# Kernel optimization log

Hardware: AMD Instinct MI355X
Metric: run time of the kernel (lower is better)

Reference implementation:

```python
import jax, jax.numpy as jnp
import numpy as np

B = 2
NUM_CLS = 20
NUM_DIM = 256
H = W = 448
FH = FW = 28
K_TOP = 25


def _l2norm(x, eps=1e-12):
    # matches torch F.normalize(dim=1): x / max(||x||, eps); zero rows stay zero
    return x / jnp.maximum(jnp.linalg.norm(x, axis=-1, keepdims=True), eps)


def setup_inputs():
    key = jax.random.key(0)
    k1, k2, k3, k4 = jax.random.split(key, 4)
    fmap = jax.random.normal(k1, (B, NUM_DIM, FH, FW), jnp.float32)
    cam = jax.random.uniform(k2, (B, NUM_CLS, H, W), jnp.float32)
    cls_label = jax.random.randint(k3, (B, NUM_CLS), 0, 2).astype(jnp.float32)
    proj_weight = jax.random.normal(k4, (NUM_CLS, NUM_DIM), jnp.float32) * 0.02
    feature_contrast = jnp.zeros((NUM_CLS, NUM_DIM), jnp.float32)
    return {"fmap": fmap, "cam": cam, "cls_label": cls_label,
            "proj_weight": proj_weight, "feature_contrast": feature_contrast,
            "hig_thre": 0.7, "low_thre": 0.25, "bg_thre": 0.5}


def _forward(fmap, cam, cls_label, proj_weight, feature_contrast, hig_thre, low_thre, bg_thre):
    b, c, h, w = cam.shape
    d = fmap.shape[1]
    dt = fmap.dtype

    # ---- pseudo-label generation (vectorized over b,h,w) ----
    valid_cam = cls_label[:, :, None, None] * cam                       # [B,C,H,W]
    top2_v, top2_i = jax.lax.top_k(jnp.moveaxis(valid_cam, 1, -1), 2)   # [B,H,W,2]
    top1, second = top2_v[..., 0], top2_v[..., 1]
    pseudo = top2_i[..., 0] + 1
    pseudo = jnp.where(top1 < hig_thre, 255, pseudo)
    pseudo = jnp.where(top1 < low_thre, 0, pseudo)
    pseudo = jnp.where(top1 < bg_thre, 0, pseudo)
    pseudo = jnp.where((top1 - second < 0.3) & (top1 > hig_thre), 255, pseudo)

    # ---- upsample features (bilinear, align_corners=False) ----
    fmap_up = jax.image.resize(fmap, (b, d, h, w), 'bilinear')
    fmap_flat = fmap_up.reshape(b, d, h * w)                            # [B,D,HW]
    pseudo_flat = pseudo.reshape(b, h * w)                              # [B,HW]

    # ---- per-class features, both branches computed densely then selected ----
    cls_ids = jnp.arange(c) + 1
    mask = (pseudo_flat[:, None, :] == cls_ids[None, :, None]).astype(dt)  # [B,C,HW]
    counts = mask.sum(-1)                                                  # [B,C]
    feat_mask = jnp.einsum('bcp,bdp->bcd', mask, fmap_flat) / jnp.maximum(counts, 1.0)[:, :, None]
    _, top_idx = jax.lax.top_k(valid_cam.reshape(b, c, h * w), K_TOP)      # [B,C,25]
    gathered = jnp.take_along_axis(fmap_flat[:, None, :, :], top_idx[:, :, None, :], axis=-1)  # [B,C,D,25]
    feat_topk = gathered.mean(-1)                                          # [B,C,D]
    present = cls_label > 0.5                                              # [B,C] bool
    fsm = jnp.where((counts == 0.0)[:, :, None], feat_topk, feat_mask) * present[:, :, None]

    eye_f = jnp.eye(c, dtype=dt)
    eye_b = jnp.eye(c, dtype=bool)

    # ---- sequential per-sample loop (EMA memory bank carried across batch) ----
    def step(carry, xs):
        fc, loss_cls, loss_ccf = carry
        fsm_i, present_i = xs                                    # [C,D], [C]
        fsm_n = _l2norm(fsm_i)
        fc_n = _l2norm(jax.lax.stop_gradient(fc))
        cos = jnp.clip(jnp.abs(fsm_n @ fc_n.T), 1e-5, 1.0 - 1e-5)  # [C,C]
        ident = jnp.diag(present_i.astype(dt))
        loss_ccf = loss_ccf - (ident * jnp.log(cos) + (1.0 - ident) * jnp.log1p(-cos)).mean()
        off_max = jnp.where(eye_b, -jnp.inf, cos).max(axis=1)      # max over j != c
        qualify = present_i & (off_max < 0.6)                      # [C] bool
        p = jax.nn.softmax(fsm_i @ proj_weight.T, axis=-1)         # [C,C]
        logp = jnp.maximum(jnp.log(p), -100.0)
        log1mp = jnp.maximum(jnp.log1p(-p), -100.0)
        term = -(eye_f * logp + (1.0 - eye_f) * log1mp).mean(axis=-1)  # BCE(softmax, onehot) per class
        loss_cls = loss_cls + jnp.sum(jnp.where(qualify, term, 0.0))
        n = qualify.sum().astype(dt)
        loss_cls = jnp.where(n > 0, loss_cls / jnp.maximum(n, 1.0), loss_cls)
        fc = jnp.where(qualify[:, None], 0.95 * fc + 0.05 * jax.lax.stop_gradient(fsm_i), fc)
        return (fc, loss_cls, loss_ccf), None

    zero = jnp.asarray(0.0, dt)
    (_, loss_cls, loss_ccf), _ = jax.lax.scan(step, (feature_contrast, zero, zero), (fsm, present))
    return loss_ccf + loss_cls


def reference(fmap, cam, cls_label, proj_weight, feature_contrast, hig_thre, low_thre, bg_thre):
    return _forward(fmap, cam, cls_label, proj_weight, feature_contrast, hig_thre, low_thre, bg_thre)
```

## Files before the change

### kernel.cpp

```cpp
#include <hip/hip_runtime.h>
#include <cstdint>

#define HW 200704
#define IMG_W 448
#define NCLS 20
#define NDIM 256
#define NB2 784
#define LK 260

#define ASYNC_COPY4(gp, lp)                                                    \
  __builtin_amdgcn_global_load_lds(                                            \
      (const __attribute__((address_space(1))) void*)(gp),                     \
      (__attribute__((address_space(3))) void*)(lp), 4, 0, 0)

__global__ __launch_bounds__(256) void k_front(const float* __restrict__ fmap,
                                               float* __restrict__ fmapT,
                                               const float* __restrict__ cam,
                                               const float* __restrict__ cls_label,
                                               const float* __restrict__ hig_p,
                                               const float* __restrict__ low_p,
                                               const float* __restrict__ bg_p,
                                               float* __restrict__ W) {
  __shared__ float sT[NCLS][256];
  int tid = threadIdx.x;

  if (blockIdx.x >= 2 * NB2) {
    float (*tile)[33] = (float (*)[33]) & sT[0][0];
    int blk = blockIdx.x - 2 * NB2;
    int b = blk / 200;
    int t = blk % 200;
    int dT = t / 25, sT2 = t % 25;
    int ty = tid >> 5, tx = tid & 31;
#pragma unroll
    for (int r = 0; r < 4; ++r) {
      int d = dT * 32 + ty + r * 8;
      int s = sT2 * 32 + tx;
      if (s < 784) tile[ty + r * 8][tx] = fmap[((size_t)(b * 256 + d)) * 784 + s];
    }
    __syncthreads();
#pragma unroll
    for (int r = 0; r < 4; ++r) {
      int s = sT2 * 32 + ty + r * 8;
      int d = dT * 32 + tx;
      if (s < 784) fmapT[((size_t)(b * 784 + s)) * 256 + d] = tile[tx][ty + r * 8];
    }
    return;
  }

  int b = blockIdx.x / NB2;
  int blkInB = blockIdx.x % NB2;
  int pix0 = blkInB * 256;
  int wave = tid >> 6, lane = tid & 63;

  bool pres = (lane < NCLS) && (cls_label[b * NCLS + lane] != 0.0f);
  unsigned long long pm = __ballot(pres);
  unsigned mask = (unsigned)(pm & 0xFFFFFu);
  int np = __popc(mask);
  const float* camb = cam + (size_t)b * NCLS * HW + pix0 + wave * 64 + lane;

  {
    unsigned m = mask;
    for (int k = 0; k < np; ++k) {
      int c = __builtin_ctz(m); m &= m - 1u;
      ASYNC_COPY4(camb + (size_t)c * HW, &sT[k][wave * 64]);
    }
  }
  __builtin_amdgcn_s_waitcnt(0);

  float top1 = -1.0f, sec = -1.0f;
  int cls1 = 0;
  {
    unsigned m = mask;
    for (int k = 0; k < np; ++k) {
      int c = __builtin_ctz(m); m &= m - 1u;
      float x = sT[k][tid];
      bool gt = x > top1;
      sec = gt ? top1 : fmaxf(sec, fminf(x, top1));
      cls1 = gt ? c : cls1;
      top1 = gt ? x : top1;
    }
  }
  if (np < NCLS) sec = fmaxf(sec, 0.0f);
  float hig = hig_p[0], low = low_p[0], bg = bg_p[0];
  int pix = pix0 + tid;
  int ps = cls1 + 1;
  if (top1 < hig) ps = 255;
  if (top1 < low) ps = 0;
  if (top1 < bg)  ps = 0;
  if ((top1 - sec < 0.3f) && (top1 > hig)) ps = 255;
  if (ps >= 1 && ps <= NCLS) {
    int cls = ps - 1;
    int y = pix / IMG_W, x = pix % IMG_W;
    float sy = (y + 0.5f) * 0.0625f - 0.5f; sy = fminf(fmaxf(sy, 0.0f), 27.0f);
    float sx = (x + 0.5f) * 0.0625f - 0.5f; sx = fminf(fmaxf(sx, 0.0f), 27.0f);
    int fy0 = (int)sy, fx0 = (int)sx;
    int fy1 = min(fy0 + 1, 27), fx1 = min(fx0 + 1, 27);
    float wy = sy - (float)fy0, wx = sx - (float)fx0;
    float* Wb = W + (size_t)(b * NCLS + cls) * 784;
    atomicAdd(&Wb[fy0 * 28 + fx0], (1.0f - wy) * (1.0f - wx));
    atomicAdd(&Wb[fy0 * 28 + fx1], (1.0f - wy) * wx);
    atomicAdd(&Wb[fy1 * 28 + fx0], wy * (1.0f - wx));
    atomicAdd(&Wb[fy1 * 28 + fx1], wy * wx);
  }
}

__global__ __launch_bounds__(512) void k_feat(const float* __restrict__ fmapT,
                                              const float* __restrict__ cam,
                                              const float* __restrict__ Wg,
                                              const float* __restrict__ cls_label,
                                              float* __restrict__ P,
                                              float* __restrict__ S,
                                              float* __restrict__ cntW) {
  __shared__ float sW[784];
  __shared__ float sH[2][256];
  __shared__ float sRed[8];
  __shared__ float sCntf;
  __shared__ float wv[8]; __shared__ int wi[8];
  __shared__ float selV; __shared__ int selI;
  __shared__ int sTop[25];
  int bc = blockIdx.x >> 2, part = blockIdx.x & 3;
  int b = bc / NCLS;
  int tid = threadIdx.x;
  int dim = tid & 255, h = tid >> 8;
  if (cls_label[bc] == 0.0f) return;

  for (int s = tid; s < 784; s += 512) sW[s] = Wg[(size_t)bc * 784 + s];
  __syncthreads();
  {
    float cs = sW[tid >= 512 ? 0 : tid];
    cs = (tid < 512) ? sW[tid] : 0.0f;
    if (tid < 272) cs += sW[tid + 512];
    for (int off = 32; off > 0; off >>= 1) cs += __shfl_xor(cs, off, 64);
    if ((tid & 63) == 0) sRed[tid >> 6] = cs;
    __syncthreads();
    if (tid == 0) {
      float s = 0.0f;
      for (int w = 0; w < 8; ++w) s += sRed[w];
      sCntf = s;
    }
    __syncthreads();
  }
  float cntf = sCntf;
  const float* fT = fmapT + (size_t)b * 784 * 256;

  if (cntf > 0.0f) {
    int s0 = part * 196;
    if (h == 0) {
      float a0 = 0.0f, a1 = 0.0f;
      for (int s = s0; s < s0 + 196; s += 4) {
        a0 += sW[s]     * fT[(size_t)(s)     * 256 + dim];
        a1 += sW[s + 1] * fT[(size_t)(s + 1) * 256 + dim];
      }
      sH[0][dim] = a0 + a1;
    } else {
      float a2 = 0.0f, a3 = 0.0f;
      for (int s = s0; s < s0 + 196; s += 4) {
        a2 += sW[s + 2] * fT[(size_t)(s + 2) * 256 + dim];
        a3 += sW[s + 3] * fT[(size_t)(s + 3) * 256 + dim];
      }
      sH[1][dim] = a2 + a3;
    }
    __syncthreads();
    if (tid < 256)
      P[(size_t)(bc * 4 + part) * 256 + tid] = sH[0][tid] + sH[1][tid];
    if (part == 0 && tid == 0) cntW[bc] = cntf;
  } else if (part == 0) {
    if (tid == 0) cntW[bc] = 0.0f;
    const float* camc = cam + (size_t)bc * HW;
    float lastV = 3.0e38f; int lastI = -1;
    for (int r = 0; r < 25; ++r) {
      float bv = -1.0e30f; int bi = 0x7fffffff;
      for (int p = tid; p < HW; p += 512) {
        float vv2 = camc[p];
        if (((vv2 < lastV) || (vv2 == lastV && p > lastI)) &&
            ((vv2 > bv) || (vv2 == bv && p < bi))) { bv = vv2; bi = p; }
      }
      for (int off = 32; off > 0; off >>= 1) {
        float ov = __shfl_xor(bv, off, 64);
        int   oi = __shfl_xor(bi, off, 64);
        if (ov > bv || (ov == bv && oi < bi)) { bv = ov; bi = oi; }
      }
      if ((tid & 63) == 0) { wv[tid >> 6] = bv; wi[tid >> 6] = bi; }
      __syncthreads();
      if (tid == 0) {
        for (int w = 1; w < 8; ++w)
          if (wv[w] > bv || (wv[w] == bv && wi[w] < bi)) { bv = wv[w]; bi = wi[w]; }
        selV = bv; selI = bi; sTop[r] = bi;
      }
      __syncthreads();
      lastV = selV; lastI = selI;
    }
    if (tid < 256) {
      float at = 0.0f;
      for (int r = 0; r < 25; ++r) {
        int p = sTop[r];
        int y = p / IMG_W, x = p % IMG_W;
        float sy = (y + 0.5f) * 0.0625f - 0.5f; sy = fminf(fmaxf(sy, 0.0f), 27.0f);
        float sx = (x + 0.5f) * 0.0625f - 0.5f; sx = fminf(fmaxf(sx, 0.0f), 27.0f);
        int fy0 = (int)sy, fx0 = (int)sx;
        int fy1 = min(fy0 + 1, 27), fx1 = min(fx0 + 1, 27);
        float wy = sy - (float)fy0, wx = sx - (float)fx0;
        at += (1.0f - wy) * (1.0f - wx) * fT[(size_t)(fy0 * 28 + fx0) * 256 + tid]
            + (1.0f - wy) * wx          * fT[(size_t)(fy0 * 28 + fx1) * 256 + tid]
            + wy          * (1.0f - wx) * fT[(size_t)(fy1 * 28 + fx0) * 256 + tid]
            + wy          * wx          * fT[(size_t)(fy1 * 28 + fx1) * 256 + tid];
      }
      S[(size_t)bc * 256 + tid] = at * (1.0f / 25.0f);
    }
  }
}

__global__ __launch_bounds__(1024) void k_loss(const float* __restrict__ P,
                                               const float* __restrict__ S,
                                               const float* __restrict__ cntW,
                                               const float* __restrict__ cls_label,
                                               const float* __restrict__ proj_w,
                                               const float* __restrict__ fc_init,
                                               float* __restrict__ out) {
  __shared__ float sFsm[2][NCLS * LK];
  __shared__ float sFc[NCLS * LK], sPw[NCLS * LK];
  __shared__ float sLogit[2][400], sCos[400];
  __shared__ float sBCE[2][NCLS], sRow[NCLS];
  __shared__ float sNormI[2][NCLS], sNormC[NCLS];
  __shared__ int   sZI[2][NCLS], sZC[NCLS], sQual[NCLS];
  __shared__ float sPres[2][NCLS];
  __shared__ float sScal[2];
  int tid = threadIdx.x;

  for (int idx = tid; idx < 2 * NCLS * NDIM; idx += 1024) {
    int bc = idx >> 8, d = idx & 255;
    float v = 0.0f;
    if (cls_label[bc] != 0.0f) {
      float c = cntW[bc];
      if (c > 0.0f) {
        const float* p = P + (size_t)bc * 1024 + d;
        v = ((p[0] + p[256]) + (p[512] + p[768])) / fmaxf(c, 1.0f);
      } else {
        v = S[(size_t)bc * 256 + d];
      }
    }
    sFsm[bc / NCLS][(bc % NCLS) * LK + d] = v;
  }
  for (int idx = tid; idx < NCLS * NDIM; idx += 1024) {
    int r = idx >> 8, d = idx & 255;
    sFc[r * LK + d] = fc_init[idx];
    sPw[r * LK + d] = proj_w[idx];
  }
  if (tid < 40) sPres[tid / NCLS][tid % NCLS] = cls_label[tid];
  if (tid == 0) { sScal[0] = 0.0f; sScal[1] = 0.0f; }
  __syncthreads();

  if (tid < 800) {
    int b = tid / 400, pi = tid % 400;
    int i = pi / NCLS, j = pi % NCLS;
    const float* ra = &sFsm[b][i * LK];
    const float* rb = &sPw[j * LK];
    float a0 = 0, a1 = 0, a2 = 0, a3 = 0, a4 = 0, a5 = 0, a6 = 0, a7 = 0;
    for (int d = 0; d < 256; d += 16) {
      float4 x0 = *(const float4*)&ra[d],      y0 = *(const float4*)&rb[d];
      float4 x1 = *(const float4*)&ra[d + 4],  y1 = *(const float4*)&rb[d + 4];
      float4 x2 = *(const float4*)&ra[d + 8],  y2 = *(const float4*)&rb[d + 8];
      float4 x3 = *(const float4*)&ra[d + 12], y3 = *(const float4*)&rb[d + 12];
      a0 += x0.x * y0.x + x0.y * y0.y;  a1 += x0.z * y0.z + x0.w * y0.w;
      a2 += x1.x * y1.x + x1.y * y1.y;  a3 += x1.z * y1.z + x1.w * y1.w;
      a4 += x2.x * y2.x + x2.y * y2.y;  a5 += x2.z * y2.z + x2.w * y2.w;
      a6 += x3.x * y3.x + x3.y * y3.y;  a7 += x3.z * y3.z + x3.w * y3.w;
    }
    sLogit[b][pi] = ((a0 + a1) + (a2 + a3)) + ((a4 + a5) + (a6 + a7));
  }
  __syncthreads();

  {
    int g = tid >> 3, sub = tid & 7;
    if (g < 60) {
      const float* row = (g < 40) ? &sFsm[g / NCLS][(g % NCLS) * LK] : &sFc[(g - 40) * LK];
      float a0 = 0.0f, a1 = 0.0f, a2 = 0.0f, a3 = 0.0f;
      int d0 = sub * 32;
#pragma unroll
      for (int d = d0; d < d0 + 32; d += 8) {
        float4 x = *(const float4*)&row[d];
        float4 y = *(const float4*)&row[d + 4];
        a0 += x.x * x.x + x.y * x.y;
        a1 += x.z * x.z + x.w * x.w;
        a2 += y.x * y.x + y.y * y.y;
        a3 += y.z * y.z + y.w * y.w;
      }
      float s = (a0 + a1) + (a2 + a3);
      s += __shfl_xor(s, 1, 64);
      s += __shfl_xor(s, 2, 64);
      s += __shfl_xor(s, 4, 64);
      if (sub == 0) {
        if (g < 40) { sNormI[g / NCLS][g % NCLS] = fmaxf(sqrtf(s), 1e-12f); sZI[g / NCLS][g % NCLS] = (s == 0.0f); }
        else { sNormC[g - 40] = fmaxf(sqrtf(s), 1e-12f); sZC[g - 40] = (s == 0.0f); }
      }
    }
  }
  __syncthreads();

  {
    int team = tid >> 5, jj = tid & 31;
    for (int r = team; r < 40; r += 32) {
      int b = r / NCLS, i = r % NCLS;
      float l = (jj < NCLS) ? sLogit[b][i * NCLS + jj] : -3.0e38f;
      float m = l;
#pragma unroll
      for (int off = 1; off < 32; off <<= 1) m = fmaxf(m, __shfl_xor(m, off, 64));
      float e = (jj < NCLS) ? expf(l - m) : 0.0f;
      float sS = e;
#pragma unroll
      for (int off = 1; off < 32; off <<= 1) sS += __shfl_xor(sS, off, 64);
      float term = 0.0f;
      if (jj < NCLS) {
        float p = e / sS;
        term = (jj == i) ? fmaxf(logf(p), -100.0f) : fmaxf(log1pf(-p), -100.0f);
      }
#pragma unroll
      for (int off = 1; off < 32; off <<= 1) term += __shfl_xor(term, off, 64);
      if (jj == 0) sBCE[b][i] = -term / 20.0f;
    }
  }
  __syncthreads();

  for (int b = 0; b < 2; ++b) {
    if (b == 1) {
      int g = tid >> 3, sub = tid & 7;
      if (g < NCLS) {
        const float* row = &sFc[g * LK];
        float a0 = 0.0f, a1 = 0.0f, a2 = 0.0f, a3 = 0.0f;
        int d0 = sub * 32;
#pragma unroll
        for (int d = d0; d < d0 + 32; d += 8) {
          float4 x = *(const float4*)&row[d];
          float4 y = *(const float4*)&row[d + 4];
          a0 += x.x * x.x + x.y * x.y;
          a1 += x.z * x.z + x.w * x.w;
          a2 += y.x * y.x + y.y * y.y;
          a3 += y.z * y.z + y.w * y.w;
        }
        float s = (a0 + a1) + (a2 + a3);
        s += __shfl_xor(s, 1, 64);
        s += __shfl_xor(s, 2, 64);
        s += __shfl_xor(s, 4, 64);
        if (sub == 0) { sNormC[g] = fmaxf(sqrtf(s), 1e-12f); sZC[g] = (s == 0.0f); }
      }
      __syncthreads();
    }
    {
      int pair = tid >> 1, sub = tid & 1;
      if (pair < 400) {
        int i = pair / NCLS, j = pair % NCLS;
        float c0;
        if (sZI[b][i] || sZC[j]) c0 = 0.0f;
        else {
          const float* ra = &sFsm[b][i * LK];
          const float* rb = &sFc[j * LK];
          float a0 = 0.0f, a1 = 0.0f, a2 = 0.0f, a3 = 0.0f;
          int d0 = sub * 128;
          for (int d = d0; d < d0 + 128; d += 8) {
            float4 x  = *(const float4*)&ra[d];
            float4 y  = *(const float4*)&rb[d];
            float4 x2 = *(const float4*)&ra[d + 4];
            float4 y2 = *(const float4*)&rb[d + 4];
            a0 += x.x * y.x + x.y * y.y;
            a1 += x.z * y.z + x.w * y.w;
            a2 += x2.x * y2.x + x2.y * y2.y;
            a3 += x2.z * y2.z + x2.w * y2.w;
          }
          float acc = (a0 + a1) + (a2 + a3);
          acc += __shfl_xor(acc, 1, 64);
          c0 = fabsf(acc / (sNormI[b][i] * sNormC[j]));
        }
        if (sub == 0) sCos[pair] = fminf(fmaxf(c0, 1e-5f), 1.0f - 1e-5f);
      }
    }
    __syncthreads();
    {
      int i = tid >> 5, jj = tid & 31;
      if (i < NCLS) {
        float pres = (sPres[b][i] > 0.5f) ? 1.0f : 0.0f;
        float contrib = 0.0f, omv = -3.0e38f;
        if (jj < NCLS) {
          float c0 = sCos[i * NCLS + jj];
          float ident = (jj == i) ? pres : 0.0f;
          contrib = ident * logf(c0) + (1.0f - ident) * log1pf(-c0);
          if (jj != i) omv = c0;
        }
#pragma unroll
        for (int off = 1; off < 32; off <<= 1) {
          contrib += __shfl_xor(contrib, off, 64);
          omv = fmaxf(omv, __shfl_xor(omv, off, 64));
        }
        if (jj == 0) { sRow[i] = contrib; sQual[i] = (pres > 0.5f && omv < 0.6f) ? 1 : 0; }
      }
    }
    __syncthreads();
    if (tid == 0) {
      float s = 0.0f;
      for (int r = 0; r < NCLS; ++r) s += sRow[r];
      sScal[0] -= s / 400.0f;
      float add = 0.0f; int nq = 0;
      for (int r = 0; r < NCLS; ++r) if (sQual[r]) { add += sBCE[b][r]; nq++; }
      float lc = sScal[1] + add;
      if (nq > 0) lc = lc / fmaxf((float)nq, 1.0f);
      sScal[1] = lc;
    }
    for (int idx = tid; idx < NCLS * NDIM; idx += 1024) {
      int r = idx >> 8, d = idx & 255;
      if (sQual[r]) sFc[r * LK + d] = 0.95f * sFc[r * LK + d] + 0.05f * sFsm[b][r * LK + d];
    }
    __syncthreads();
  }
  if (tid == 0) out[0] = sScal[0] + sScal[1];
}

extern "C" void kernel_launch(void* const* d_in, const int* in_sizes, int n_in,
                              void* d_out, int out_size, void* d_ws, size_t ws_size,
                              hipStream_t stream) {
  const float* fmap      = (const float*)d_in[0];
  const float* cam       = (const float*)d_in[1];
  const float* cls_label = (const float*)d_in[2];
  const float* proj_w    = (const float*)d_in[3];
  const float* fc_init   = (const float*)d_in[4];
  const float* hig       = (const float*)d_in[5];
  const float* low       = (const float*)d_in[6];
  const float* bg        = (const float*)d_in[7];
  float* out = (float*)d_out;

  char* ws = (char*)d_ws;
  float* W     = (float*)(ws);
  float* cntW  = (float*)(ws + 125440);
  float* P     = (float*)(ws + 125600);
  float* S     = (float*)(ws + 289440);
  float* fmapT = (float*)(ws + 330400);

  hipMemsetAsync(ws, 0, 125440, stream);
  k_front<<<2 * NB2 + 400,  256, 0, stream>>>(fmap, fmapT, cam, cls_label,
                                              hig, low, bg, W);
  k_feat <<<          160,  512, 0, stream>>>(fmapT, cam, W, cls_label, P, S, cntW);
  k_loss <<<            1, 1024, 0, stream>>>(P, S, cntW, cls_label, proj_w, fc_init, out);
}
```

Measured before the change: 127.6 us.

## Split single-block loss kernel into parallel per-row precompute and tiny final reduction

The single-block loss kernel is replaced by a 40-block k_pre kernel, one block per (batch, class) row, plus a small k_final kernel. k_pre computes the softmax BCE term and the cosines for that row. For batch 1 it computes cosines against both the original and the updated feature_contrast rows, so the sequential EMA dependency becomes a per-row select in k_final. The aim is to spread the dot-product work over many CUs instead of one workgroup. The cost is an extra kernel launch, redundant per-block loads of fc and proj_weight, and extra global round-trips.

```diff
diff --git a/kernel.cpp b/kernel.cpp
--- a/kernel.cpp
+++ b/kernel.cpp
@@ -210,25 +210,32 @@
   }
 }
 
-__global__ __launch_bounds__(1024) void k_loss(const float* __restrict__ P,
-                                               const float* __restrict__ S,
-                                               const float* __restrict__ cntW,
-                                               const float* __restrict__ cls_label,
-                                               const float* __restrict__ proj_w,
-                                               const float* __restrict__ fc_init,
-                                               float* __restrict__ out) {
-  __shared__ float sFsm[2][NCLS * LK];
+__global__ __launch_bounds__(256) void k_pre(const float* __restrict__ P,
+                                             const float* __restrict__ S,
+                                             const float* __restrict__ cntW,
+                                             const float* __restrict__ cls_label,
+                                             const float* __restrict__ proj_w,
+                                             const float* __restrict__ fc_init,
+                                             float* __restrict__ BCEg,
+                                             float* __restrict__ COS0,
+                                             float* __restrict__ COS1V) {
+  __shared__ float sOwn[LK];
   __shared__ float sFc[NCLS * LK], sPw[NCLS * LK];
-  __shared__ float sLogit[2][400], sCos[400];
-  __shared__ float sBCE[2][NCLS], sRow[NCLS];
-  __shared__ float sNormI[2][NCLS], sNormC[NCLS];
-  __shared__ int   sZI[2][NCLS], sZC[NCLS], sQual[NCLS];
-  __shared__ float sPres[2][NCLS];
-  __shared__ float sScal[2];
+  __shared__ float sF0[NCLS * LK], sFv[NCLS * LK];
+  __shared__ float sLog[NCLS];
+  __shared__ float sNC[NCLS], sNCv[NCLS];
+  __shared__ int   sZC[NCLS], sZCv[NCLS];
+  __shared__ float sNI[1]; __shared__ int sZI[1];
   int tid = threadIdx.x;
-
-  for (int idx = tid; idx < 2 * NCLS * NDIM; idx += 1024) {
-    int bc = idx >> 8, d = idx & 255;
+  int b = blockIdx.x / NCLS, i = blockIdx.x % NCLS;
+
+  for (int idx = tid; idx < NCLS * NDIM; idx += 256) {
+    int r = idx >> 8, d = idx & 255;
+    sFc[r * LK + d] = fc_init[idx];
+    sPw[r * LK + d] = proj_w[idx];
+  }
+  {
+    int bc = b * NCLS + i, d = tid;
     float v = 0.0f;
     if (cls_label[bc] != 0.0f) {
       float c = cntW[bc];
@@ -239,22 +246,86 @@
         v = S[(size_t)bc * 256 + d];
       }
     }
-    sFsm[bc / NCLS][(bc % NCLS) * LK + d] = v;
-  }
-  for (int idx = tid; idx < NCLS * NDIM; idx += 1024) {
-    int r = idx >> 8, d = idx & 255;
-    sFc[r * LK + d] = fc_init[idx];
-    sPw[r * LK + d] = proj_w[idx];
-  }
-  if (tid < 40) sPres[tid / NCLS][tid % NCLS] = cls_label[tid];
-  if (tid == 0) { sScal[0] = 0.0f; sScal[1] = 0.0f; }
+    sOwn[d] = v;
+  }
+  if (b == 1) {
+    for (int idx = tid; idx < NCLS * NDIM; idx += 256) {
+      int bc = idx >> 8, d = idx & 255;
+      float v = 0.0f;
+      if (cls_label[bc] != 0.0f) {
+        float c = cntW[bc];
+        if (c > 0.0f) {
+          const float* p = P + (size_t)bc * 1024 + d;
+          v = ((p[0] + p[256]) + (p[512] + p[768])) / fmaxf(c, 1.0f);
+        } else {
+          v = S[(size_t)bc * 256 + d];
+        }
+      }
+      sF0[bc * LK + d] = v;
+    }
+  }
   __syncthreads();
-
-  if (tid < 800) {
-    int b = tid / 400, pi = tid % 400;
-    int i = pi / NCLS, j = pi % NCLS;
-    const float* ra = &sFsm[b][i * LK];
-    const float* rb = &sPw[j * LK];
+  if (b == 1) {
+    for (int idx = tid; idx < NCLS * NDIM; idx += 256) {
+      int r = idx >> 8, d = idx & 255;
+      sFv[r * LK + d] = 0.95f * sFc[r * LK + d] + 0.05f * sF0[r * LK + d];
+    }
+    __syncthreads();
+  }
+
+  {
+    int g = tid >> 3, sub = tid & 7;
+    if (g <= 20) {
+      const float* row = (g < 20) ? &sFc[g * LK] : sOwn;
+      float a0 = 0.0f, a1 = 0.0f, a2 = 0.0f, a3 = 0.0f;
+      int d0 = sub * 32;
+#pragma unroll
+      for (int d = d0; d < d0 + 32; d += 8) {
+        float4 x = *(const float4*)&row[d];
+        float4 y = *(const float4*)&row[d + 4];
+        a0 += x.x * x.x + x.y * x.y;
+        a1 += x.z * x.z + x.w * x.w;
+        a2 += y.x * y.x + y.y * y.y;
+        a3 += y.z * y.z + y.w * y.w;
+      }
+      float s = (a0 + a1) + (a2 + a3);
+      s += __shfl_xor(s, 1, 64);
+      s += __shfl_xor(s, 2, 64);
+      s += __shfl_xor(s, 4, 64);
+      if (sub == 0) {
+        if (g < 20) { sNC[g] = fmaxf(sqrtf(s), 1e-12f); sZC[g] = (s == 0.0f); }
+        else        { sNI[0] = fmaxf(sqrtf(s), 1e-12f); sZI[0] = (s == 0.0f); }
+      }
+    }
+  }
+  __syncthreads();
+  if (b == 1) {
+    int g = tid >> 3, sub = tid & 7;
+    if (g < 20) {
+      const float* row = &sFv[g * LK];
+      float a0 = 0.0f, a1 = 0.0f, a2 = 0.0f, a3 = 0.0f;
+      int d0 = sub * 32;
+#pragma unroll
+      for (int d = d0; d < d0 + 32; d += 8) {
+        float4 x = *(const float4*)&row[d];
+        float4 y = *(const float4*)&row[d + 4];
+        a0 += x.x * x.x + x.y * x.y;
+        a1 += x.z * x.z + x.w * x.w;
+        a2 += y.x * y.x + y.y * y.y;
+        a3 += y.z * y.z + y.w * y.w;
+      }
+      float s = (a0 + a1) + (a2 + a3);
+      s += __shfl_xor(s, 1, 64);
+      s += __shfl_xor(s, 2, 64);
+      s += __shfl_xor(s, 4, 64);
+      if (sub == 0) { sNCv[g] = fmaxf(sqrtf(s), 1e-12f); sZCv[g] = (s == 0.0f); }
+    }
+    __syncthreads();
+  }
+
+  if (tid < NCLS) {
+    const float* ra = sOwn;
+    const float* rb = &sPw[tid * LK];
     float a0 = 0, a1 = 0, a2 = 0, a3 = 0, a4 = 0, a5 = 0, a6 = 0, a7 = 0;
     for (int d = 0; d < 256; d += 16) {
       float4 x0 = *(const float4*)&ra[d],      y0 = *(const float4*)&rb[d];
@@ -266,114 +337,112 @@
       a4 += x2.x * y2.x + x2.y * y2.y;  a5 += x2.z * y2.z + x2.w * y2.w;
       a6 += x3.x * y3.x + x3.y * y3.y;  a7 += x3.z * y3.z + x3.w * y3.w;
     }
-    sLogit[b][pi] = ((a0 + a1) + (a2 + a3)) + ((a4 + a5) + (a6 + a7));
+    sLog[tid] = ((a0 + a1) + (a2 + a3)) + ((a4 + a5) + (a6 + a7));
   }
   __syncthreads();
 
-  {
-    int g = tid >> 3, sub = tid & 7;
-    if (g < 60) {
-      const float* row = (g < 40) ? &sFsm[g / NCLS][(g % NCLS) * LK] : &sFc[(g - 40) * LK];
+  if (tid < 32) {
+    int jj = tid;
+    float l = (jj < NCLS) ? sLog[jj] : -3.0e38f;
+    float m = l;
+#pragma unroll
+    for (int off = 1; off < 32; off <<= 1) m = fmaxf(m, __shfl_xor(m, off, 64));
+    float e = (jj < NCLS) ? expf(l - m) : 0.0f;
+    float sS = e;
+#pragma unroll
+    for (int off = 1; off < 32; off <<= 1) sS += __shfl_xor(sS, off, 64);
+    float term = 0.0f;
+    if (jj < NCLS) {
+      float p = e / sS;
+      term = (jj == i) ? fmaxf(logf(p), -100.0f) : fmaxf(log1pf(-p), -100.0f);
+    }
+#pragma unroll
+    for (int off = 1; off < 32; off <<= 1) term += __shfl_xor(term, off, 64);
+    if (jj == 0) BCEg[b * NCLS + i] = -term / 20.0f;
+  }
+  if (tid >= 64 && tid < 64 + 2 * NCLS) {
+    int j = (tid - 64) >> 1, sub = tid & 1;
+    float c0;
+    if (sZI[0] || sZC[j]) c0 = 0.0f;
+    else {
+      const float* ra = sOwn;
+      const float* rb = &sFc[j * LK];
       float a0 = 0.0f, a1 = 0.0f, a2 = 0.0f, a3 = 0.0f;
-      int d0 = sub * 32;
-#pragma unroll
-      for (int d = d0; d < d0 + 32; d += 8) {
-        float4 x = *(const float4*)&row[d];
-        float4 y = *(const float4*)&row[d + 4];
-        a0 += x.x * x.x + x.y * x.y;
-        a1 += x.z * x.z + x.w * x.w;
-        a2 += y.x * y.x + y.y * y.y;
-        a3 += y.z * y.z + y.w * y.w;
-      }
-      float s = (a0 + a1) + (a2 + a3);
-      s += __shfl_xor(s, 1, 64);
-      s += __shfl_xor(s, 2, 64);
-      s += __shfl_xor(s, 4, 64);
-      if (sub == 0) {
-        if (g < 40) { sNormI[g / NCLS][g % NCLS] = fmaxf(sqrtf(s), 1e-12f); sZI[g / NCLS][g % NCLS] = (s == 0.0f); }
-        else { sNormC[g - 40] = fmaxf(sqrtf(s), 1e-12f); sZC[g - 40] = (s == 0.0f); }
-      }
-    }
-  }
-  __syncthreads();
-
-  {
-    int team = tid >> 5, jj = tid & 31;
-    for (int r = team; r < 40; r += 32) {
-      int b = r / NCLS, i = r % NCLS;
-      float l = (jj < NCLS) ? sLogit[b][i * NCLS + jj] : -3.0e38f;
-      float m = l;
-#pragma unroll
-      for (int off = 1; off < 32; off <<= 1) m = fmaxf(m, __shfl_xor(m, off, 64));
-      float e = (jj < NCLS) ? expf(l - m) : 0.0f;
-      float sS = e;
-#pragma unroll
-      for (int off = 1; off < 32; off <<= 1) sS += __shfl_xor(sS, off, 64);
-      float term = 0.0f;
-      if (jj < NCLS) {
-        float p = e / sS;
-        term = (jj == i) ? fmaxf(logf(p), -100.0f) : fmaxf(log1pf(-p), -100.0f);
-      }
-#pragma unroll
-      for (int off = 1; off < 32; off <<= 1) term += __shfl_xor(term, off, 64);
-      if (jj == 0) sBCE[b][i] = -term / 20.0f;
-    }
-  }
+      int d0 = sub * 128;
+      for (int d = d0; d < d0 + 128; d += 8) {
+        float4 x  = *(const float4*)&ra[d];
+        float4 y  = *(const float4*)&rb[d];
+        float4 x2 = *(const float4*)&ra[d + 4];
+        float4 y2 = *(const float4*)&rb[d + 4];
+        a0 += x.x * y.x + x.y * y.y;
+        a1 += x.z * y.z + x.w * y.w;
+        a2 += x2.x * y2.x + x2.y * y2.y;
+        a3 += x2.z * y2.z + x2.w * y2.w;
+      }
+      float acc = (a0 + a1) + (a2 + a3);
+      acc += __shfl_xor(acc, 1, 64);
+      c0 = fabsf(acc / (sNI[0] * sNC[j]));
+    }
+    if (sub == 0) {
+      float cv = fminf(fmaxf(c0, 1e-5f), 1.0f - 1e-5f);
+      if (b == 0) COS0[i * NCLS + j] = cv;
+      else        COS1V[i * NCLS + j] = cv;
+    }
+  }
+  if (b == 1 && tid >= 128 && tid < 128 + 2 * NCLS) {
+    int j = (tid - 128) >> 1, sub = tid & 1;
+    float c0;
+    if (sZI[0] || sZCv[j]) c0 = 0.0f;
+    else {
+      const float* ra = sOwn;
+      const float* rb = &sFv[j * LK];
+      float a0 = 0.0f, a1 = 0.0f, a2 = 0.0f, a3 = 0.0f;
+      int d0 = sub * 128;
+      for (int d = d0; d < d0 + 128; d += 8) {
+        float4 x  = *(const float4*)&ra[d];
+        float4 y  = *(const float4*)&rb[d];
+        float4 x2 = *(const float4*)&ra[d + 4];
+        float4 y2 = *(const float4*)&rb[d + 4];
+        a0 += x.x * y.x + x.y * y.y;
+        a1 += x.z * y.z + x.w * y.w;
+        a2 += x2.x * y2.x + x2.y * y2.y;
+        a3 += x2.z * y2.z + x2.w * y2.w;
+      }
+      float acc = (a0 + a1) + (a2 + a3);
+      acc += __shfl_xor(acc, 1, 64);
+      c0 = fabsf(acc / (sNI[0] * sNCv[j]));
+    }
+    if (sub == 0)
+      COS1V[400 + i * NCLS + j] = fminf(fmaxf(c0, 1e-5f), 1.0f - 1e-5f);
+  }
+}
+
+__global__ __launch_bounds__(1024) void k_final(const float* __restrict__ BCEg,
+                                                const float* __restrict__ COS0,
+                                                const float* __restrict__ COS1V,
+                                                const float* __restrict__ cls_label,
+                                                float* __restrict__ out) {
+  __shared__ float sCos[400];
+  __shared__ float sBCE[2][NCLS], sRow[NCLS];
+  __shared__ int   sQual[NCLS];
+  __shared__ float sPres[2][NCLS];
+  __shared__ float sScal[2];
+  int tid = threadIdx.x;
+
+  if (tid < 400) sCos[tid] = COS0[tid];
+  if (tid < 40) { sBCE[tid / NCLS][tid % NCLS] = BCEg[tid];
+                  sPres[tid / NCLS][tid % NCLS] = cls_label[tid]; }
+  if (tid == 0) { sScal[0] = 0.0f; sScal[1] = 0.0f; }
   __syncthreads();
 
   for (int b = 0; b < 2; ++b) {
     if (b == 1) {
-      int g = tid >> 3, sub = tid & 7;
-      if (g < NCLS) {
-        const float* row = &sFc[g * LK];
-        float a0 = 0.0f, a1 = 0.0f, a2 = 0.0f, a3 = 0.0f;
-        int d0 = sub * 32;
-#pragma unroll
-        for (int d = d0; d < d0 + 32; d += 8) {
-          float4 x = *(const float4*)&row[d];
-          float4 y = *(const float4*)&row[d + 4];
-          a0 += x.x * x.x + x.y * x.y;
-          a1 += x.z * x.z + x.w * x.w;
-          a2 += y.x * y.x + y.y * y.y;
-          a3 += y.z * y.z + y.w * y.w;
-        }
-        float s = (a0 + a1) + (a2 + a3);
-        s += __shfl_xor(s, 1, 64);
-        s += __shfl_xor(s, 2, 64);
-        s += __shfl_xor(s, 4, 64);
-        if (sub == 0) { sNormC[g] = fmaxf(sqrtf(s), 1e-12f); sZC[g] = (s == 0.0f); }
+      if (tid < 400) {
+        int j = tid % NCLS;
+        sCos[tid] = sQual[j] ? COS1V[400 + tid] : COS1V[tid];
       }
       __syncthreads();
     }
-    {
-      int pair = tid >> 1, sub = tid & 1;
-      if (pair < 400) {
-        int i = pair / NCLS, j = pair % NCLS;
-        float c0;
-        if (sZI[b][i] || sZC[j]) c0 = 0.0f;
-        else {
-          const float* ra = &sFsm[b][i * LK];
-          const float* rb = &sFc[j * LK];
-          float a0 = 0.0f, a1 = 0.0f, a2 = 0.0f, a3 = 0.0f;
-          int d0 = sub * 128;
-          for (int d = d0; d < d0 + 128; d += 8) {
-            float4 x  = *(const float4*)&ra[d];
-            float4 y  = *(const float4*)&rb[d];
-            float4 x2 = *(const float4*)&ra[d + 4];
-            float4 y2 = *(const float4*)&rb[d + 4];
-            a0 += x.x * y.x + x.y * y.y;
-            a1 += x.z * y.z + x.w * y.w;
-            a2 += x2.x * y2.x + x2.y * y2.y;
-            a3 += x2.z * y2.z + x2.w * y2.w;
-          }
-          float acc = (a0 + a1) + (a2 + a3);
-          acc += __shfl_xor(acc, 1, 64);
-          c0 = fabsf(acc / (sNormI[b][i] * sNormC[j]));
-        }
-        if (sub == 0) sCos[pair] = fminf(fmaxf(c0, 1e-5f), 1.0f - 1e-5f);
-      }
-    }
-    __syncthreads();
     {
       int i = tid >> 5, jj = tid & 31;
       if (i < NCLS) {
@@ -403,10 +472,6 @@
       float lc = sScal[1] + add;
       if (nq > 0) lc = lc / fmaxf((float)nq, 1.0f);
       sScal[1] = lc;
-    }
-    for (int idx = tid; idx < NCLS * NDIM; idx += 1024) {
-      int r = idx >> 8, d = idx & 255;
-      if (sQual[r]) sFc[r * LK + d] = 0.95f * sFc[r * LK + d] + 0.05f * sFsm[b][r * LK + d];
     }
     __syncthreads();
   }
@@ -432,10 +497,15 @@
   float* P     = (float*)(ws + 125600);
   float* S     = (float*)(ws + 289440);
   float* fmapT = (float*)(ws + 330400);
+  float* BCEg  = (float*)(ws + 1936032);
+  float* COS0v = (float*)(ws + 1936192);
+  float* COS1V = (float*)(ws + 1937792);
 
   hipMemsetAsync(ws, 0, 125440, stream);
   k_front<<<2 * NB2 + 400,  256, 0, stream>>>(fmap, fmapT, cam, cls_label,
                                               hig, low, bg, W);
   k_feat <<<          160,  512, 0, stream>>>(fmapT, cam, W, cls_label, P, S, cntW);
-  k_loss <<<            1, 1024, 0, stream>>>(P, S, cntW, cls_label, proj_w, fc_init, out);
+  k_pre  <<<   2 * NCLS,    256, 0, stream>>>(P, S, cntW, cls_label, proj_w,
+                                              fc_init, BCEg, COS0v, COS1V);
+  k_final<<<            1, 1024, 0, stream>>>(BCEg, COS0v, COS1V, cls_label, out);
 }
```

Result: faster. 121.0 us (-5.2%).
